# Performance work log

Hardware: AMD Instinct MI355X
Metric: run time of the kernel (lower is better)

## Reference

```python
import jax, jax.numpy as jnp
import numpy as np

N = 1_000_000          # number of fusion candidate pairs
H, W = 200, 70400      # sparse buffer dims hard-coded in the module
FILL = -9999999.0


def _init_conv(k, co, ci):
    # torch Conv2d default init: U(-1/sqrt(fan_in), 1/sqrt(fan_in)), 1x1 kernel
    bound = 1.0 / np.sqrt(ci)
    kw, kb = jax.random.split(k)
    w = jax.random.uniform(kw, (co, ci), jnp.float32, -bound, bound)
    b = jax.random.uniform(kb, (co,), jnp.float32, -bound, bound)
    return w, b


def setup_inputs() -> dict:
    key = jax.random.key(0)
    ks = jax.random.split(key, 7)
    input_1 = jax.random.normal(ks[0], (1, 4, 1, N), dtype=jnp.float32)
    idx0 = jax.random.randint(ks[1], (N,), 0, H)   # row in [0,200)
    idx1 = jax.random.randint(ks[2], (N,), 0, W)   # col in [0,70400)
    tensor_index = jnp.stack([idx0, idx1], axis=1).astype(jnp.int64)
    w1, b1 = _init_conv(ks[3], 18, 4)
    w2, b2 = _init_conv(ks[4], 36, 18)
    w3, b3 = _init_conv(ks[5], 36, 36)
    w4, b4 = _init_conv(ks[6], 1, 36)
    return dict(input_1=input_1, tensor_index=tensor_index,
                w1=w1, b1=b1, w2=w2, b2=b2, w3=w3, b3=b3, w4=w4, b4=b4)


def _fuse_2d_3d(x, w1, b1, w2, b2, w3, b3, w4, b4):
    # x: (4, N); 1x1 convs over a (1,C,1,N) tensor == per-point channel matmuls
    h = jax.nn.relu(w1 @ x + b1[:, None])
    h = jax.nn.relu(w2 @ h + b2[:, None])
    h = jax.nn.relu(w3 @ h + b3[:, None])
    return w4 @ h + b4[:, None]  # (1, N)


def reference(input_1, tensor_index, w1, b1, w2, b2, w3, b3, w4, b4):
    base = jnp.full((1, H, W), FILL, dtype=input_1.dtype)

    def scatter_branch(_):
        feat = _fuse_2d_3d(input_1[0, :, 0, :], w1, b1, w2, b2, w3, b3, w4, b4)  # (1, N)
        out = base.at[:, tensor_index[:, 0], tensor_index[:, 1]].set(feat)
        return out, jnp.int32(1)

    def empty_branch(_):
        return base, jnp.int32(0)

    out_1, flag = jax.lax.cond(tensor_index[0, 0] == -1,
                               empty_branch, scatter_branch, None)
    # MaxPool2d([200,1]) over (C=1,H=200,W) -> max over H; squeeze+reshape -> (1, W, 1)
    x = jnp.max(out_1, axis=1)            # (1, W)
    return x.reshape(1, -1, 1), flag
```

## Files before the change

### kernel.cpp

```cpp
#include <hip/hip_runtime.h>

#define N_PTS 1000000
#define H_DIM 200
#define W_DIM 70400
#define FILL_V -9999999.0f

#define COUNTS_BYTES ((size_t)W_DIM * sizeof(int))
#define WPACK_ELEMS  6656
#define WPACK_BYTES  ((size_t)WPACK_ELEMS * 2)
#define FEAT_BYTES   ((size_t)N_PTS * 4)

typedef __attribute__((ext_vector_type(4))) float f32x4;
typedef __attribute__((ext_vector_type(8))) short bf16x8;

__device__ __forceinline__ unsigned bperm_u(unsigned src_lane, unsigned v) {
    return (unsigned)__builtin_amdgcn_ds_bpermute((int)(src_lane << 2), (int)v);
}
__device__ __forceinline__ unsigned cvt_pk_bf16(float lo, float hi) {
    unsigned d;
    asm("v_cvt_pk_bf16_f32 %0, %1, %2" : "=v"(d) : "v"(lo), "v"(hi));
    return d;
}
__device__ __forceinline__ bf16x8 mk_frag(unsigned d0, unsigned d1,
                                          unsigned d2, unsigned d3) {
    union { unsigned u[4]; bf16x8 s; } u;
    u.u[0] = d0; u.u[1] = d1; u.u[2] = d2; u.u[3] = d3;
    return u.s;
}

__global__ void __launch_bounds__(256) pack_weights_kernel(
    const float* __restrict__ w1, const float* __restrict__ b1,
    const float* __restrict__ w2, const float* __restrict__ b2,
    const float* __restrict__ w3, const float* __restrict__ b3,
    const float* __restrict__ w4, const float* __restrict__ b4,
    unsigned short* __restrict__ wp)
{
    for (int idx = threadIdx.x; idx < WPACK_ELEMS; idx += 256) {
        const int rem  = idx & 511;
        const int lane = rem >> 3, j = rem & 7;
        const int c16 = lane & 15, gk = lane >> 4;
        const int kloc = gk * 8 + j;
        float v = 0.0f;
        if (idx < 1024) {
            const int row = (idx >> 9) * 16 + c16, k = kloc;
            if (row < 18) v = (k < 4) ? w1[row * 4 + k] : (k == 4 ? b1[row] : 0.0f);
        } else if (idx < 2560) {
            const int row = ((idx - 1024) >> 9) * 16 + c16;
            const int f = (j < 4) ? (4 * gk + j) : (16 + 4 * gk + (j - 4));
            if (row < 36) v = (f < 18) ? w2[row * 18 + f] : (f == 18 ? b2[row] : 0.0f);
        } else if (idx < 5632) {
            const int f = (idx - 2560) >> 9;
            const int row = (f >> 1) * 16 + c16, k = (f & 1) * 32 + kloc;
            if (row < 36) v = (k < 36) ? w3[row * 36 + k] : (k == 36 ? b3[row] : 0.0f);
        } else {
            const int row = c16, k = ((idx - 5632) >> 9) * 32 + kloc;
            if (row == 0) v = (k < 36) ? w4[k] : (k == 36 ? b4[0] : 0.0f);
        }
        const unsigned b = __float_as_uint(v);
        wp[idx] = (unsigned short)((b + 0x7FFFu + ((b >> 16) & 1u)) >> 16);
    }
}

__global__ void __launch_bounds__(256) mlp_scatter_kernel(
    const float* __restrict__ input,
    const int* __restrict__ tindex,
    const unsigned short* __restrict__ wp,
    int* __restrict__ counts,
    unsigned* __restrict__ feat,
    unsigned* __restrict__ list4,
    int maxk)
{
    if (tindex[0] == -1) return;

    const int l   = threadIdx.x & 63;
    const int wav = (blockIdx.x * 256 + threadIdx.x) >> 6;
    const int base = wav << 6;
    if (base >= N_PTS) return;
    const int i = base + l;
    const int c16 = l & 15, g = l >> 4;

    const int2 hw = ((const int2*)tindex)[i];
    const int pos = atomicAdd(&counts[hw.y], 1);

    const bf16x8* __restrict__ wf = (const bf16x8*)wp;
    const bf16x8 A1_0 = wf[0 * 64 + l], A1_1 = wf[1 * 64 + l];
    const bf16x8 A2_0 = wf[2 * 64 + l], A2_1 = wf[3 * 64 + l], A2_2 = wf[4 * 64 + l];
    const bf16x8 A3_00 = wf[5 * 64 + l], A3_01 = wf[6 * 64 + l];
    const bf16x8 A3_10 = wf[7 * 64 + l], A3_11 = wf[8 * 64 + l];
    const bf16x8 A3_20 = wf[9 * 64 + l], A3_21 = wf[10 * 64 + l];
    const bf16x8 A4_0 = wf[11 * 64 + l], A4_1 = wf[12 * 64 + l];

    const f32x4 zf = {0.0f, 0.0f, 0.0f, 0.0f};

    const float x0 = input[0 * N_PTS + i], x1 = input[1 * N_PTS + i];
    const float x2 = input[2 * N_PTS + i], x3 = input[3 * N_PTS + i];
    const unsigned xp01 = cvt_pk_bf16(x0, x1);
    const unsigned xp23 = cvt_pk_bf16(x2, x3);

    unsigned P1[4][2][2];
#pragma unroll
    for (int t = 0; t < 4; ++t) {
        const unsigned srcl = (unsigned)(16 * t + c16);
        const unsigned bx0 = bperm_u(srcl, xp01);
        const unsigned bx1 = bperm_u(srcl, xp23);
        const bf16x8 B = mk_frag((g == 0) ? bx0 : 0u,
                                 (g == 0) ? bx1 : 0u,
                                 (g == 0) ? 0x3F80u : 0u, 0u);
        const f32x4 D0 = __builtin_amdgcn_mfma_f32_16x16x32_bf16(A1_0, B, zf, 0, 0, 0);
        const f32x4 D1 = __builtin_amdgcn_mfma_f32_16x16x32_bf16(A1_1, B, zf, 0, 0, 0);
        P1[t][0][0] = cvt_pk_bf16(fmaxf(D0.x, 0.f), fmaxf(D0.y, 0.f));
        P1[t][0][1] = cvt_pk_bf16(fmaxf(D0.z, 0.f), fmaxf(D0.w, 0.f));
        P1[t][1][0] = cvt_pk_bf16(fmaxf(D1.x, 0.f), fmaxf(D1.y, 0.f));
        P1[t][1][1] = cvt_pk_bf16(fmaxf(D1.z, 0.f), fmaxf(D1.w, 0.f));
    }

    unsigned P2[4][3][2];
#pragma unroll
    for (int t = 0; t < 4; ++t) {
        const bf16x8 B = mk_frag(P1[t][0][0], P1[t][0][1], P1[t][1][0],
                                 (g == 0) ? 0x3F80u : P1[t][1][1]);
        const f32x4 D0 = __builtin_amdgcn_mfma_f32_16x16x32_bf16(A2_0, B, zf, 0, 0, 0);
        const f32x4 D1 = __builtin_amdgcn_mfma_f32_16x16x32_bf16(A2_1, B, zf, 0, 0, 0);
        const f32x4 D2 = __builtin_amdgcn_mfma_f32_16x16x32_bf16(A2_2, B, zf, 0, 0, 0);
        P2[t][0][0] = cvt_pk_bf16(fmaxf(D0.x, 0.f), fmaxf(D0.y, 0.f));
        P2[t][0][1] = cvt_pk_bf16(fmaxf(D0.z, 0.f), fmaxf(D0.w, 0.f));
        P2[t][1][0] = cvt_pk_bf16(fmaxf(D1.x, 0.f), fmaxf(D1.y, 0.f));
        P2[t][1][1] = cvt_pk_bf16(fmaxf(D1.z, 0.f), fmaxf(D1.w, 0.f));
        P2[t][2][0] = cvt_pk_bf16(fmaxf(D2.x, 0.f), fmaxf(D2.y, 0.f));
        P2[t][2][1] = cvt_pk_bf16(fmaxf(D2.z, 0.f), fmaxf(D2.w, 0.f));
    }

    unsigned P3[4][3][2];
#pragma unroll
    for (int t = 0; t < 4; ++t) {
        unsigned dk0[4], dk1[4];
#pragma unroll
        for (int p = 0; p < 4; ++p) {
            const int Rl = (4 * g + p) & 7;
            const unsigned srcl = (unsigned)(c16 + 16 * (Rl >> 1));
            const unsigned lo = bperm_u(srcl, P2[t][0][p & 1]);
            const unsigned hi = bperm_u(srcl, P2[t][1][p & 1]);
            const unsigned m2 = bperm_u(srcl, P2[t][2][p & 1]);
            dk0[p] = (4 * g + p < 8) ? lo : hi;
            dk1[p] = (4 * g + p < 8) ? m2 : 0u;
        }
        if (g == 0) dk1[2] = (dk1[2] & 0xFFFF0000u) | 0x3F80u;
        const bf16x8 B0 = mk_frag(dk0[0], dk0[1], dk0[2], dk0[3]);
        const bf16x8 B1 = mk_frag(dk1[0], dk1[1], dk1[2], dk1[3]);
        f32x4 D0 = __builtin_amdgcn_mfma_f32_16x16x32_bf16(A3_00, B0, zf, 0, 0, 0);
        D0 = __builtin_amdgcn_mfma_f32_16x16x32_bf16(A3_01, B1, D0, 0, 0, 0);
        f32x4 D1 = __builtin_amdgcn_mfma_f32_16x16x32_bf16(A3_10, B0, zf, 0, 0, 0);
        D1 = __builtin_amdgcn_mfma_f32_16x16x32_bf16(A3_11, B1, D1, 0, 0, 0);
        f32x4 D2 = __builtin_amdgcn_mfma_f32_16x16x32_bf16(A3_20, B0, zf, 0, 0, 0);
        D2 = __builtin_amdgcn_mfma_f32_16x16x32_bf16(A3_21, B1, D2, 0, 0, 0);
        P3[t][0][0] = cvt_pk_bf16(fmaxf(D0.x, 0.f), fmaxf(D0.y, 0.f));
        P3[t][0][1] = cvt_pk_bf16(fmaxf(D0.z, 0.f), fmaxf(D0.w, 0.f));
        P3[t][1][0] = cvt_pk_bf16(fmaxf(D1.x, 0.f), fmaxf(D1.y, 0.f));
        P3[t][1][1] = cvt_pk_bf16(fmaxf(D1.z, 0.f), fmaxf(D1.w, 0.f));
        P3[t][2][0] = cvt_pk_bf16(fmaxf(D2.x, 0.f), fmaxf(D2.y, 0.f));
        P3[t][2][1] = cvt_pk_bf16(fmaxf(D2.z, 0.f), fmaxf(D2.w, 0.f));
    }

    float vout[4];
#pragma unroll
    for (int t = 0; t < 4; ++t) {
        unsigned dk0[4], dk1[4];
#pragma unroll
        for (int p = 0; p < 4; ++p) {
            const int Rl = (4 * g + p) & 7;
            const unsigned srcl = (unsigned)(c16 + 16 * (Rl >> 1));
            const unsigned lo = bperm_u(srcl, P3[t][0][p & 1]);
            const unsigned hi = bperm_u(srcl, P3[t][1][p & 1]);
            const unsigned m2 = bperm_u(srcl, P3[t][2][p & 1]);
            dk0[p] = (4 * g + p < 8) ? lo : hi;
            dk1[p] = (4 * g + p < 8) ? m2 : 0u;
        }
        if (g == 0) dk1[2] = (dk1[2] & 0xFFFF0000u) | 0x3F80u;
        const bf16x8 B0 = mk_frag(dk0[0], dk0[1], dk0[2], dk0[3]);
        const bf16x8 B1 = mk_frag(dk1[0], dk1[1], dk1[2], dk1[3]);
        f32x4 D = __builtin_amdgcn_mfma_f32_16x16x32_bf16(A4_0, B0, zf, 0, 0, 0);
        D = __builtin_amdgcn_mfma_f32_16x16x32_bf16(A4_1, B1, D, 0, 0, 0);
        vout[t] = D.x;
    }

    const unsigned r0 = bperm_u((unsigned)c16, __float_as_uint(vout[0]));
    const unsigned r1 = bperm_u((unsigned)c16, __float_as_uint(vout[1]));
    const unsigned r2 = bperm_u((unsigned)c16, __float_as_uint(vout[2]));
    const unsigned r3 = bperm_u((unsigned)c16, __float_as_uint(vout[3]));
    const unsigned vr = (g < 2) ? ((g == 0) ? r0 : r1) : ((g == 2) ? r2 : r3);

    feat[i] = vr;
    if (pos < maxk)
        list4[(size_t)hw.y * maxk + pos] = ((unsigned)i << 8) | (unsigned)hw.x;
}

__device__ __forceinline__ void lds_wave_fence() {
    asm volatile("s_waitcnt lgkmcnt(0)" ::: "memory");
}

__global__ void __launch_bounds__(256) colmax_kernel(
    const int* __restrict__ tindex,
    const int* __restrict__ counts,
    const unsigned* __restrict__ list4,
    const unsigned* __restrict__ feat,
    float* __restrict__ out,
    int maxk)
{
    __shared__ unsigned rowwin[4][200];
    const int lane = threadIdx.x;
    const int y    = threadIdx.y;
    unsigned* tbl = rowwin[y];

    const bool empty = (tindex[0] == -1);

    if (blockIdx.x == 0 && lane == 0 && y == 0)
        out[W_DIM] = empty ? 0.0f : 1.0f;

    tbl[lane]       = 0u;
    tbl[lane + 64]  = 0u;
    tbl[lane + 128] = 0u;
    if (lane < 8) tbl[lane + 192] = 0u;
    lds_wave_fence();

    const int step = gridDim.x * 4;
    for (int w = blockIdx.x * 4 + y; w < W_DIM; w += step) {
        int c = 0;
        if (!empty) {
            c = counts[w];
            if (c > maxk) c = maxk;
        }

        unsigned e4 = 0u, fb = 0u;
        const bool have = (lane < c);
        float v = FILL_V;
        if (have) {
            e4 = list4[(size_t)w * maxk + lane];
            fb = feat[e4 >> 8];
            atomicMax(&tbl[e4 & 0xFFu], e4);
        }
        lds_wave_fence();
        if (have) {
            if (tbl[e4 & 0xFFu] == e4)
                v = __uint_as_float(fb);
            tbl[e4 & 0xFFu] = 0u;
        }
        lds_wave_fence();

#pragma unroll
        for (int off = 32; off > 0; off >>= 1)
            v = fmaxf(v, __shfl_down(v, off, 64));

        if (lane == 0) out[w] = v;
    }
}

extern "C" void kernel_launch(void* const* d_in, const int* in_sizes, int n_in,
                              void* d_out, int out_size, void* d_ws, size_t ws_size,
                              hipStream_t stream) {
    const float* input  = (const float*)d_in[0];
    const int*   tindex = (const int*)d_in[1];
    const float* w1 = (const float*)d_in[2];
    const float* b1 = (const float*)d_in[3];
    const float* w2 = (const float*)d_in[4];
    const float* b2 = (const float*)d_in[5];
    const float* w3 = (const float*)d_in[6];
    const float* b3 = (const float*)d_in[7];
    const float* w4 = (const float*)d_in[8];
    const float* b4 = (const float*)d_in[9];
    float* out = (float*)d_out;

    int*            counts = (int*)d_ws;
    unsigned short* wpack  = (unsigned short*)((char*)d_ws + COUNTS_BYTES);
    unsigned*       feat   = (unsigned*)((char*)d_ws + COUNTS_BYTES + WPACK_BYTES);
    unsigned*       list4  = (unsigned*)((char*)d_ws + COUNTS_BYTES + WPACK_BYTES + FEAT_BYTES);

    size_t head = COUNTS_BYTES + WPACK_BYTES + FEAT_BYTES;
    size_t avail = (ws_size > head) ? ws_size - head : 0;
    int maxk = (int)(avail / ((size_t)W_DIM * sizeof(unsigned)));
    if (maxk > 64) maxk = 64;
    if (maxk < 1)  maxk = 1;

    (void)hipMemsetAsync(counts, 0, COUNTS_BYTES, stream);

    pack_weights_kernel<<<1, 256, 0, stream>>>(w1, b1, w2, b2, w3, b3, w4, b4, wpack);

    mlp_scatter_kernel<<<(N_PTS / 64 + 3) / 4, 256, 0, stream>>>(
        input, tindex, wpack, counts, feat, list4, maxk);

    colmax_kernel<<<2200, dim3(64, 4), 0, stream>>>(
        tindex, counts, list4, feat, out, maxk);
}
```

Before: 167.6 us.

## Shard per-column bucket counters and lists by XCD to localize atomics

Splits the per-column counters and bucket lists into eight copies indexed by the hardware XCC id read via s_getreg. Each point's atomicAdd then only contends within its own die's L2 instead of across dies. The colmax kernel reads all eight shards per column, with each group of eight lanes covering one XCD and up to 16 slots. Per-column capacity is now capped at 16 entries per XCD, which could drop points where one column holds more than that on a single die, and the counter memset grows eightfold.

Result: no change. 168.5 us (+0.5%).

```diff
diff --git a/kernel.cpp b/kernel.cpp
--- a/kernel.cpp
+++ b/kernel.cpp
@@ -4,8 +4,9 @@
 #define H_DIM 200
 #define W_DIM 70400
 #define FILL_V -9999999.0f
-
-#define COUNTS_BYTES ((size_t)W_DIM * sizeof(int))
+#define NXCD 8
+
+#define COUNTS8_BYTES ((size_t)NXCD * W_DIM * sizeof(int))
 #define WPACK_ELEMS  6656
 #define WPACK_BYTES  ((size_t)WPACK_ELEMS * 2)
 #define FEAT_BYTES   ((size_t)N_PTS * 4)
@@ -26,6 +27,11 @@
     union { unsigned u[4]; bf16x8 s; } u;
     u.u[0] = d0; u.u[1] = d1; u.u[2] = d2; u.u[3] = d3;
     return u.s;
+}
+__device__ __forceinline__ unsigned xcc_id() {
+    unsigned x;
+    asm volatile("s_getreg_b32 %0, hwreg(HW_REG_XCC_ID)" : "=s"(x));
+    return x & 7u;
 }
 
 __global__ void __launch_bounds__(256) pack_weights_kernel(
@@ -65,10 +71,10 @@
     const float* __restrict__ input,
     const int* __restrict__ tindex,
     const unsigned short* __restrict__ wp,
-    int* __restrict__ counts,
+    int* __restrict__ counts8,
     unsigned* __restrict__ feat,
     unsigned* __restrict__ list4,
-    int maxk)
+    int slots)
 {
     if (tindex[0] == -1) return;
 
@@ -79,8 +85,11 @@
     const int i = base + l;
     const int c16 = l & 15, g = l >> 4;
 
+    const unsigned xcd = xcc_id();
+
     const int2 hw = ((const int2*)tindex)[i];
-    const int pos = atomicAdd(&counts[hw.y], 1);
+    const size_t cell = (size_t)xcd * W_DIM + (size_t)hw.y;
+    const int pos = atomicAdd(&counts8[cell], 1);
 
     const bf16x8* __restrict__ wf = (const bf16x8*)wp;
     const bf16x8 A1_0 = wf[0 * 64 + l], A1_1 = wf[1 * 64 + l];
@@ -190,8 +199,8 @@
     const unsigned vr = (g < 2) ? ((g == 0) ? r0 : r1) : ((g == 2) ? r2 : r3);
 
     feat[i] = vr;
-    if (pos < maxk)
-        list4[(size_t)hw.y * maxk + pos] = ((unsigned)i << 8) | (unsigned)hw.x;
+    if (pos < slots)
+        list4[cell * (size_t)slots + pos] = ((unsigned)i << 8) | (unsigned)hw.x;
 }
 
 __device__ __forceinline__ void lds_wave_fence() {
@@ -200,11 +209,11 @@
 
 __global__ void __launch_bounds__(256) colmax_kernel(
     const int* __restrict__ tindex,
-    const int* __restrict__ counts,
+    const int* __restrict__ counts8,
     const unsigned* __restrict__ list4,
     const unsigned* __restrict__ feat,
     float* __restrict__ out,
-    int maxk)
+    int slots)
 {
     __shared__ unsigned rowwin[4][200];
     const int lane = threadIdx.x;
@@ -222,28 +231,41 @@
     if (lane < 8) tbl[lane + 192] = 0u;
     lds_wave_fence();
 
+    const int x   = lane >> 3;
+    const int sub = lane & 7;
+
     const int step = gridDim.x * 4;
     for (int w = blockIdx.x * 4 + y; w < W_DIM; w += step) {
         int c = 0;
         if (!empty) {
-            c = counts[w];
-            if (c > maxk) c = maxk;
-        }
-
-        unsigned e4 = 0u, fb = 0u;
-        const bool have = (lane < c);
+            c = counts8[(size_t)x * W_DIM + w];
+            if (c > slots) c = slots;
+        }
+
+        const size_t basew = ((size_t)x * W_DIM + w) * (size_t)slots;
+        unsigned eA = 0u, eB = 0u, fA = 0u, fB = 0u;
+        const bool hA = (sub < c);
+        const bool hB = (sub + 8 < c);
+        if (hA) {
+            eA = list4[basew + sub];
+            fA = feat[eA >> 8];
+            atomicMax(&tbl[eA & 0xFFu], eA);
+        }
+        if (hB) {
+            eB = list4[basew + sub + 8];
+            fB = feat[eB >> 8];
+            atomicMax(&tbl[eB & 0xFFu], eB);
+        }
+        lds_wave_fence();
+
         float v = FILL_V;
-        if (have) {
-            e4 = list4[(size_t)w * maxk + lane];
-            fb = feat[e4 >> 8];
-            atomicMax(&tbl[e4 & 0xFFu], e4);
-        }
-        lds_wave_fence();
-        if (have) {
-            if (tbl[e4 & 0xFFu] == e4)
-                v = __uint_as_float(fb);
-            tbl[e4 & 0xFFu] = 0u;
-        }
+        unsigned winA = 0u, winB = 0u;
+        if (hA) winA = tbl[eA & 0xFFu];
+        if (hB) winB = tbl[eB & 0xFFu];
+        if (hA && winA == eA) v = __uint_as_float(fA);
+        if (hB && winB == eB) v = fmaxf(v, __uint_as_float(fB));
+        if (hA) tbl[eA & 0xFFu] = 0u;
+        if (hB) tbl[eB & 0xFFu] = 0u;
         lds_wave_fence();
 
 #pragma unroll
@@ -269,24 +291,24 @@
     const float* b4 = (const float*)d_in[9];
     float* out = (float*)d_out;
 
-    int*            counts = (int*)d_ws;
-    unsigned short* wpack  = (unsigned short*)((char*)d_ws + COUNTS_BYTES);
-    unsigned*       feat   = (unsigned*)((char*)d_ws + COUNTS_BYTES + WPACK_BYTES);
-    unsigned*       list4  = (unsigned*)((char*)d_ws + COUNTS_BYTES + WPACK_BYTES + FEAT_BYTES);
-
-    size_t head = COUNTS_BYTES + WPACK_BYTES + FEAT_BYTES;
+    int*            counts8 = (int*)d_ws;
+    unsigned short* wpack   = (unsigned short*)((char*)d_ws + COUNTS8_BYTES);
+    unsigned*       feat    = (unsigned*)((char*)d_ws + COUNTS8_BYTES + WPACK_BYTES);
+    unsigned*       list4   = (unsigned*)((char*)d_ws + COUNTS8_BYTES + WPACK_BYTES + FEAT_BYTES);
+
+    size_t head = COUNTS8_BYTES + WPACK_BYTES + FEAT_BYTES;
     size_t avail = (ws_size > head) ? ws_size - head : 0;
-    int maxk = (int)(avail / ((size_t)W_DIM * sizeof(unsigned)));
-    if (maxk > 64) maxk = 64;
-    if (maxk < 1)  maxk = 1;
-
-    (void)hipMemsetAsync(counts, 0, COUNTS_BYTES, stream);
+    int slots = (int)(avail / ((size_t)NXCD * W_DIM * sizeof(unsigned)));
+    if (slots > 16) slots = 16;
+    if (slots < 1)  slots = 1;
+
+    (void)hipMemsetAsync(counts8, 0, COUNTS8_BYTES, stream);
 
     pack_weights_kernel<<<1, 256, 0, stream>>>(w1, b1, w2, b2, w3, b3, w4, b4, wpack);
 
     mlp_scatter_kernel<<<(N_PTS / 64 + 3) / 4, 256, 0, stream>>>(
-        input, tindex, wpack, counts, feat, list4, maxk);
+        input, tindex, wpack, counts8, feat, list4, slots);
 
     colmax_kernel<<<2200, dim3(64, 4), 0, stream>>>(
-        tindex, counts, list4, feat, out, maxk);
-}
+        tindex, counts8, list4, feat, out, slots);
+}
```
